# Performance work log

Hardware: AMD Instinct MI355X
Metric: run time of the kernel (lower is better)

Reference implementation:

```python
import jax, jax.numpy as jnp
import numpy as np

B, S, D, H, DH = 2, 2048, 1024, 16, 64

def setup_inputs() -> dict:
    key = jax.random.key(0)
    ks = jax.random.split(key, 9)
    sc = 0.02
    return {
        "x":  jax.random.normal(ks[0], (B, S, D), jnp.float32),
        "Wq": jax.random.normal(ks[1], (H, D, DH), jnp.float32) * sc,
        "bq": jax.random.normal(ks[2], (H, DH), jnp.float32) * sc,
        "Wk": jax.random.normal(ks[3], (H, D, DH), jnp.float32) * sc,
        "bk": jax.random.normal(ks[4], (H, DH), jnp.float32) * sc,
        "Wv": jax.random.normal(ks[5], (H, D, DH), jnp.float32) * sc,
        "bv": jax.random.normal(ks[6], (H, DH), jnp.float32) * sc,
        "Wo": jax.random.normal(ks[7], (D, D), jnp.float32) * sc,
        "bo": jax.random.normal(ks[8], (D,), jnp.float32) * sc,
    }

def reference(x, Wq, bq, Wk, bk, Wv, bv, Wo, bo):
    # Fused version of the per-head Python loop: all H heads batched.
    # q,k,v: [B,H,S,DH]
    q = jnp.einsum("bsi,hid->bhsd", x, Wq) + bq[None, :, None, :]
    k = jnp.einsum("bsi,hid->bhsd", x, Wk) + bk[None, :, None, :]
    v = jnp.einsum("bsi,hid->bhsd", x, Wv) + bv[None, :, None, :]
    scale = 1.0 / jnp.sqrt(jnp.asarray(DH, x.dtype))
    scores = jnp.einsum("bhsd,bhtd->bhst", q, k) * scale  # [B,H,S,S]
    attn = jax.nn.softmax(scores, axis=-1)
    o = jnp.einsum("bhst,bhtd->bhsd", attn, v)            # [B,H,S,DH]
    # torch.cat([head_0,...,head_{H-1}], dim=-1) -> [B,S,H*DH]
    o = jnp.transpose(o, (0, 2, 1, 3)).reshape(B, S, H * DH)
    # Dropout is identity in eval mode; final dense projection.
    return jnp.einsum("bsi,io->bso", o, Wo) + bo
```

## Files before the change

### kernel.cpp

```cpp
#include <hip/hip_runtime.h>
#include <hip/hip_bf16.h>

#define BB 2
#define SS 2048
#define DD 1024
#define HH 16
#define DHH 64

typedef __attribute__((ext_vector_type(8))) __bf16 bf16x8;
typedef __attribute__((ext_vector_type(4))) float f32x4;
typedef __attribute__((ext_vector_type(16))) float f32x16;
typedef __attribute__((ext_vector_type(4))) int i32x4;
typedef __attribute__((ext_vector_type(4))) unsigned int u32x4;

#define MFMA16 __builtin_amdgcn_mfma_f32_16x16x32_bf16
#define MFMA32 __builtin_amdgcn_mfma_f32_32x32x16_bf16

__device__ __forceinline__ unsigned short f2b(float f) {
  __hip_bfloat16 h = __float2bfloat16(f);
  unsigned short u;
  __builtin_memcpy(&u, &h, 2);
  return u;
}

__device__ __forceinline__ float b2f(unsigned short u) {
  unsigned int x = ((unsigned int)u) << 16;
  float f;
  __builtin_memcpy(&f, &x, 4);
  return f;
}

__device__ __forceinline__ float exp2_fast(float x) {
  float r;
  asm("v_exp_f32 %0, %1" : "=v"(r) : "v"(x));
  return r;
}

__device__ __forceinline__ unsigned int cvtpk_bf16(float lo_, float hi_) {
  unsigned int r;
  asm("v_cvt_pk_bf16_f32 %0, %1, %2" : "=v"(r) : "v"(lo_), "v"(hi_));
  return r;
}

__device__ __forceinline__ void gl_lds16(const void* g, void* l) {
  __builtin_amdgcn_global_load_lds((const __attribute__((address_space(1))) void*)g,
                                   (__attribute__((address_space(3))) void*)l, 16, 0, 0);
}

__global__ __launch_bounds__(256) void k_prep(const float* __restrict__ x,
                                              const float* __restrict__ Wq,
                                              const float* __restrict__ Wk,
                                              const float* __restrict__ Wv,
                                              const float* __restrict__ Wo,
                                              unsigned short* __restrict__ xb,
                                              unsigned short* __restrict__ wqkvt,
                                              unsigned short* __restrict__ wot) {
  int blk = blockIdx.x;
  if (blk < 4096) {
    int i = blk * 256 + threadIdx.x;
    float4 v = ((const float4*)x)[i];
    ushort4 o;
    o.x = f2b(v.x); o.y = f2b(v.y); o.z = f2b(v.z); o.w = f2b(v.w);
    ((ushort4*)xb)[i] = o;
    return;
  }
  __shared__ float t[32][33];
  const float* im;
  unsigned short* om;
  int R, C, c0, r0;
  if (blk < 7168) {
    int bi2 = blk - 4096;
    int z = bi2 >> 6, rem = bi2 & 63;
    im = (z < 16 ? Wq : (z < 32 ? Wk : Wv)) + (size_t)(z & 15) * DD * DHH;
    om = wqkvt + (size_t)z * DD * DHH;
    R = DD; C = DHH;
    c0 = (rem & 1) * 32; r0 = (rem >> 1) * 32;
  } else {
    int bi2 = blk - 7168;
    im = Wo; om = wot;
    R = DD; C = DD;
    c0 = (bi2 & 31) * 32; r0 = (bi2 >> 5) * 32;
  }
  int tx = threadIdx.x & 31, ty = threadIdx.x >> 5;
#pragma unroll
  for (int rr = ty; rr < 32; rr += 8)
    t[rr][tx] = im[(size_t)(r0 + rr) * C + c0 + tx];
  __syncthreads();
#pragma unroll
  for (int rr = ty; rr < 32; rr += 8)
    om[(size_t)(c0 + rr) * R + r0 + tx] = f2b(t[tx][rr]);
}

__global__ __launch_bounds__(256) void k_qkv(const unsigned short* __restrict__ A,
                                             const unsigned short* __restrict__ Wt,
                                             const float* __restrict__ bq,
                                             const float* __restrict__ bk,
                                             const float* __restrict__ bv,
                                             unsigned short* __restrict__ Qb,
                                             unsigned short* __restrict__ Kb,
                                             unsigned short* __restrict__ Vtb) {
  __shared__ __align__(16) unsigned short SMEM[2 * 12288];
  int tid = threadIdx.x;
  int w = tid >> 6, l = tid & 63, lr = l & 15, lg = l >> 4;
  int col0 = blockIdx.x * 64, row0 = blockIdx.y * 128;
  int sel = col0 >> 10;
  bool vsel = (sel == 2);
  const float* biasp = sel == 0 ? bq : (sel == 1 ? bk : bv);
  unsigned short* outp = sel == 0 ? Qb : Kb;
  float qscale = sel == 0 ? 0.18033688011112042f : 1.0f;

  int r8 = l >> 3, c8 = l & 7;
  const unsigned short* Ab = A + (size_t)(row0 + w * 32 + r8) * DD + c8 * 8;
  const unsigned short* Bb = Wt + (size_t)(col0 + w * 16 + r8) * DD + c8 * 8;

  f32x4 zero = {0.f, 0.f, 0.f, 0.f};
  f32x4 acc[2][4];
#pragma unroll
  for (int m = 0; m < 2; m++)
#pragma unroll
    for (int n = 0; n < 4; n++) acc[m][n] = zero;

#define QKV_STAGE(T) do { \
    unsigned short* buf_ = SMEM + ((T) & 1) * 12288; \
    int k0_ = (T) * 64; \
    _Pragma("unroll") \
    for (int c = 0; c < 4; c++) \
      gl_lds16(Ab + (size_t)c * 8 * DD + k0_, (char*)buf_ + (w * 32 + c * 8) * 128); \
    _Pragma("unroll") \
    for (int c = 0; c < 2; c++) \
      gl_lds16(Bb + (size_t)c * 8 * DD + k0_, (char*)(buf_ + 8192) + (w * 16 + c * 8) * 128); \
  } while (0)

  QKV_STAGE(0);
  __syncthreads();

  for (int t = 0; t < 16; t++) {
    const unsigned short* As = SMEM + (t & 1) * 12288;
    const unsigned short* Bs = As + 8192;
    if (t + 1 < 16) QKV_STAGE(t + 1);
#pragma unroll
    for (int kk = 0; kk < 2; kk++) {
      bf16x8 af[2], bfr[4];
#pragma unroll
      for (int m = 0; m < 2; m++)
        af[m] = *(const bf16x8*)&As[(w * 32 + m * 16 + lr) * 64 + kk * 32 + lg * 8];
#pragma unroll
      for (int n = 0; n < 4; n++)
        bfr[n] = *(const bf16x8*)&Bs[(n * 16 + lr) * 64 + kk * 32 + lg * 8];
      if (!vsel) {
#pragma unroll
        for (int m = 0; m < 2; m++)
#pragma unroll
          for (int n = 0; n < 4; n++)
            acc[m][n] = MFMA16(af[m], bfr[n], acc[m][n], 0, 0, 0);
      } else {
#pragma unroll
        for (int m = 0; m < 2; m++)
#pragma unroll
          for (int n = 0; n < 4; n++)
            acc[m][n] = MFMA16(bfr[n], af[m], acc[m][n], 0, 0, 0);
      }
    }
    __syncthreads();
  }
#undef QKV_STAGE

  unsigned short* Ts = SMEM;
  if (!vsel) {
#pragma unroll
    for (int n = 0; n < 4; n++) {
      int cl = n * 16 + lr;
      float bias = biasp[(col0 + cl) & 1023];
#pragma unroll
      for (int m = 0; m < 2; m++) {
#pragma unroll
        for (int j = 0; j < 4; j++) {
          int sl = w * 32 + m * 16 + lg * 4 + j;
          Ts[sl * 72 + cl] = f2b((acc[m][n][j] + bias) * qscale);
        }
      }
    }
    __syncthreads();
    int trow = tid >> 3, tc = tid & 7;
#pragma unroll
    for (int pass = 0; pass < 4; pass++) {
      int sl = pass * 32 + trow;
      int c0l = tc * 8;
      i32x4 v = *(const i32x4*)&Ts[sl * 72 + c0l];
      int c = col0 + c0l;
      int hh = (c >> 6) & 15, d = c & 63;
      int row = row0 + sl;
      int b = row >> 11, s = row & 2047;
      *(i32x4*)(outp + ((size_t)(b * HH + hh) * SS + s) * DHH + d) = v;
    }
  } else {
#pragma unroll
    for (int n = 0; n < 4; n++) {
#pragma unroll
      for (int j = 0; j < 4; j++) {
        int cl = n * 16 + lg * 4 + j;
        float bias = bv[((col0 & 1023) + cl) & 1023];
#pragma unroll
        for (int m = 0; m < 2; m++) {
          int sl = w * 32 + m * 16 + lr;
          Ts[cl * 136 + sl] = f2b(acc[m][n][j] + bias);
        }
      }
    }
    __syncthreads();
    int trow = tid >> 4, tc = tid & 15;
    int b = row0 >> 11, s0 = row0 & 2047;
#pragma unroll
    for (int pass = 0; pass < 4; pass++) {
      int cl = pass * 16 + trow;
      int s8 = tc * 8;
      i32x4 v = *(const i32x4*)&Ts[cl * 136 + s8];
      int cg = (col0 & 1023) + cl;
      *(i32x4*)(Vtb + (size_t)(b * 1024 + cg) * SS + s0 + s8) = v;
    }
  }
}

__global__ __launch_bounds__(256) void k_proj(const unsigned short* __restrict__ A,
                                              const unsigned short* __restrict__ Wt,
                                              const float* __restrict__ bo,
                                              float* __restrict__ out) {
  __shared__ __align__(16) unsigned short SMEM[2 * 8192];
  int tid = threadIdx.x;
  int w = tid >> 6, l = tid & 63, lr = l & 15, lg = l >> 4;
  int col0 = blockIdx.x * 64, row0 = blockIdx.y * 64;

  int r8 = l >> 3, c8 = l & 7;
  const unsigned short* Ab = A + (size_t)(row0 + w * 16 + r8) * DD + c8 * 8;
  const unsigned short* Bb = Wt + (size_t)(col0 + w * 16 + r8) * DD + c8 * 8;

  f32x4 zero = {0.f, 0.f, 0.f, 0.f};
  f32x4 acc[4];
#pragma unroll
  for (int n = 0; n < 4; n++) acc[n] = zero;

#define PROJ_STAGE(T) do { \
    unsigned short* buf_ = SMEM + ((T) & 1) * 8192; \
    int k0_ = (T) * 64; \
    _Pragma("unroll") \
    for (int c = 0; c < 2; c++) { \
      gl_lds16(Ab + (size_t)c * 8 * DD + k0_, (char*)buf_ + (w * 16 + c * 8) * 128); \
      gl_lds16(Bb + (size_t)c * 8 * DD + k0_, (char*)(buf_ + 4096) + (w * 16 + c * 8) * 128); \
    } \
  } while (0)

  PROJ_STAGE(0);
  __syncthreads();

  for (int t = 0; t < 16; t++) {
    const unsigned short* As = SMEM + (t & 1) * 8192;
    const unsigned short* Bs = As + 4096;
    if (t + 1 < 16) PROJ_STAGE(t + 1);
#pragma unroll
    for (int kk = 0; kk < 2; kk++) {
      bf16x8 af = *(const bf16x8*)&As[(w * 16 + lr) * 64 + kk * 32 + lg * 8];
      bf16x8 bfr[4];
#pragma unroll
      for (int n = 0; n < 4; n++)
        bfr[n] = *(const bf16x8*)&Bs[(n * 16 + lr) * 64 + kk * 32 + lg * 8];
#pragma unroll
      for (int n = 0; n < 4; n++)
        acc[n] = MFMA16(af, bfr[n], acc[n], 0, 0, 0);
    }
    __syncthreads();
  }
#undef PROJ_STAGE

#pragma unroll
  for (int n = 0; n < 4; n++) {
    int c = col0 + n * 16 + lr;
    float bias = bo[c];
#pragma unroll
    for (int j = 0; j < 4; j++) {
      int row = row0 + w * 16 + lg * 4 + j;
      out[(size_t)row * DD + c] = acc[n][j] + bias;
    }
  }
}

#define QT 128
#define KVB 64

__global__ __launch_bounds__(256, 4) void k_attn(const unsigned short* __restrict__ Q,
                                                 const unsigned short* __restrict__ K,
                                                 const unsigned short* __restrict__ Vt,
                                                 unsigned short* __restrict__ Opart,
                                                 float* __restrict__ lse) {
  __shared__ __align__(16) char sm[32768];

  int tid = threadIdx.x;
  int w = tid >> 6, lane = tid & 63;
  int q32 = lane & 31, hi = lane >> 5;
  int r8 = lane >> 3, c8 = lane & 7;
  int cg = c8 ^ r8;

  int n = blockIdx.x;
  int bh = ((n & 7) << 2) | ((n >> 3) & 3);
  int rest = n >> 5;
  int q0 = (rest & 15) * QT;
  int chunk = rest >> 4;
  int kvbase = chunk * (SS / 2);

  const unsigned short* Qm = Q + (size_t)bh * SS * DHH;
  const unsigned short* Km = K + (size_t)bh * SS * DHH;
  const unsigned short* Vm = Vt + (size_t)bh * DHH * SS;

  bf16x8 qf[4];
  {
    const unsigned short* qrow = Qm + (size_t)(q0 + w * 32 + q32) * DHH + hi * 8;
#pragma unroll
    for (int ks = 0; ks < 4; ks++)
      qf[ks] = *(const bf16x8*)(qrow + ks * 16);
  }

#pragma unroll
  for (int c = 0; c < 2; c++) {
    int rr = w * 16 + c * 8 + r8;
    gl_lds16(Km + (size_t)(kvbase + rr) * DHH + cg * 8, sm + (w * 16 + c * 8) * 128);
    gl_lds16(Vm + (size_t)rr * SS + kvbase + cg * 8, sm + 16384 + (w * 16 + c * 8) * 128);
  }
  __syncthreads();

  f32x16 oacc0 = {}, oacc1 = {};
  float m_ = -1e30f, l_ = 0.f;
  const int swq = (q32 & 7) << 4;

  for (int t = 0; t < SS / 2 / KVB; t++) {
    const char* Kc = sm + (t & 1) * 8192;
    const char* Vc = sm + 16384 + (t & 1) * 8192;

    if (t + 1 < SS / 2 / KVB) {
      int kv0 = kvbase + (t + 1) * KVB;
      char* kd = sm + ((t + 1) & 1) * 8192;
      char* vd = sm + 16384 + ((t + 1) & 1) * 8192;
#pragma unroll
      for (int c = 0; c < 2; c++) {
        int rr = w * 16 + c * 8 + r8;
        gl_lds16(Km + (size_t)(kv0 + rr) * DHH + cg * 8, kd + (w * 16 + c * 8) * 128);
        gl_lds16(Vm + (size_t)rr * SS + kv0 + cg * 8, vd + (w * 16 + c * 8) * 128);
      }
    }

    f32x16 p0 = {}, p1 = {};
    __builtin_amdgcn_s_setprio(1);
#pragma unroll
    for (int ks = 0; ks < 4; ks++) {
      int co = (ks * 32 + hi * 16) ^ swq;
      bf16x8 kf0 = *(const bf16x8*)(Kc + q32 * 128 + co);
      bf16x8 kf1 = *(const bf16x8*)(Kc + (32 + q32) * 128 + co);
      p0 = MFMA32(kf0, qf[ks], p0, 0, 0, 0);
      p1 = MFMA32(kf1, qf[ks], p1, 0, 0, 0);
    }
    __builtin_amdgcn_s_setprio(0);

    float t8[8];
#pragma unroll
    for (int r = 0; r < 8; r++)
      t8[r] = fmaxf(fmaxf(p0[r], p0[r + 8]), fmaxf(p1[r], p1[r + 8]));
#pragma unroll
    for (int r = 0; r < 4; r++) t8[r] = fmaxf(t8[r], t8[r + 4]);
    float tmax = fmaxf(fmaxf(t8[0], t8[1]), fmaxf(t8[2], t8[3]));
    tmax = fmaxf(tmax, __shfl_xor(tmax, 32));

    if (__any(tmax > m_ + 8.0f)) {
      float nm = fmaxf(m_, tmax);
      float al = exp2_fast(m_ - nm);
      m_ = nm; l_ *= al;
#pragma unroll
      for (int r = 0; r < 16; r++) { oacc0[r] *= al; oacc1[r] *= al; }
    }

#pragma unroll
    for (int r = 0; r < 16; r++) p0[r] = exp2_fast(p0[r] - m_);
#pragma unroll
    for (int r = 0; r < 16; r++) p1[r] = exp2_fast(p1[r] - m_);
    float s8[8];
#pragma unroll
    for (int r = 0; r < 8; r++) s8[r] = (p0[r] + p0[r + 8]) + (p1[r] + p1[r + 8]);
#pragma unroll
    for (int r = 0; r < 4; r++) s8[r] += s8[r + 4];
    l_ += ((s8[0] + s8[1]) + (s8[2] + s8[3]));

    __builtin_amdgcn_s_setprio(1);
    u32x4 pa;
#define MKPA(PB, u) do { \
    unsigned int a0 = cvtpk_bf16(PB[8*(u)+0], PB[8*(u)+1]); \
    unsigned int a1 = cvtpk_bf16(PB[8*(u)+2], PB[8*(u)+3]); \
    unsigned int b0 = cvtpk_bf16(PB[8*(u)+4], PB[8*(u)+5]); \
    unsigned int b1 = cvtpk_bf16(PB[8*(u)+6], PB[8*(u)+7]); \
    asm("v_permlane32_swap_b32 %0, %1" : "+v"(a0), "+v"(b0)); \
    asm("v_permlane32_swap_b32 %0, %1" : "+v"(a1), "+v"(b1)); \
    pa[0] = a0; pa[1] = a1; pa[2] = b0; pa[3] = b1; \
  } while (0)
#define PVSTEP(s) do { \
    bf16x8 pf = *(bf16x8*)&pa; \
    bf16x8 vf0 = *(const bf16x8*)(Vc + q32 * 128 + (((s) * 32 + hi * 16) ^ swq)); \
    bf16x8 vf1 = *(const bf16x8*)(Vc + (32 + q32) * 128 + (((s) * 32 + hi * 16) ^ swq)); \
    oacc0 = MFMA32(vf0, pf, oacc0, 0, 0, 0); \
    oacc1 = MFMA32(vf1, pf, oacc1, 0, 0, 0); \
  } while (0)
    MKPA(p0, 0); PVSTEP(0);
    MKPA(p0, 1); PVSTEP(1);
    MKPA(p1, 0); PVSTEP(2);
    MKPA(p1, 1); PVSTEP(3);
#undef MKPA
#undef PVSTEP
    __builtin_amdgcn_s_setprio(0);

    __syncthreads();
  }

  l_ += __shfl_xor(l_, 32);
  float invl = 1.0f / l_;
  float lsev = m_ + __log2f(l_);
  __syncthreads();
  unsigned short* Os = (unsigned short*)sm;
  int rowq = w * 32 + q32;
#pragma unroll
  for (int r = 0; r < 16; r++) {
    int d = (r & 3) + 8 * (r >> 2) + 4 * hi;
    Os[rowq * 72 + d] = f2b(oacc0[r] * invl);
    Os[rowq * 72 + 32 + d] = f2b(oacc1[r] * invl);
  }
  if (hi == 0) lse[((size_t)chunk * 32 + bh) * SS + q0 + rowq] = lsev;
  __syncthreads();
#pragma unroll
  for (int i = 0; i < 4; i++) {
    int ci = tid + i * 256;
    int r = ci >> 3, c = ci & 7;
    i32x4 v = *(const i32x4*)&Os[r * 72 + c * 8];
    *(i32x4*)(Opart + (((size_t)chunk * 32 + bh) * SS + q0 + r) * DHH + c * 8) = v;
  }
}

__global__ __launch_bounds__(256) void k_comb(const unsigned short* __restrict__ Opart,
                                              const float* __restrict__ lse,
                                              unsigned short* __restrict__ Ocat) {
  int g = blockIdx.x * 256 + threadIdx.x;
  int row = g >> 3;
  int d8 = (g & 7) * 8;
  int bh = row >> 11, q = row & 2047;
  int bi = bh >> 4, h = bh & 15;
  float e0 = lse[row], e1 = lse[BB * HH * SS + row];
  float mx = fmaxf(e0, e1);
  float w0 = exp2_fast(e0 - mx), w1 = exp2_fast(e1 - mx);
  float inv = 1.0f / (w0 + w1);
  w0 *= inv; w1 *= inv;
  const unsigned short* P0 = Opart + (size_t)row * DHH + d8;
  const unsigned short* P1 = P0 + (size_t)BB * HH * SS * DHH;
  ushort4 a0 = *(const ushort4*)P0, a1 = *(const ushort4*)(P0 + 4);
  ushort4 b0 = *(const ushort4*)P1, b1 = *(const ushort4*)(P1 + 4);
  ushort4 o0, o1;
  o0.x = f2b(w0 * b2f(a0.x) + w1 * b2f(b0.x));
  o0.y = f2b(w0 * b2f(a0.y) + w1 * b2f(b0.y));
  o0.z = f2b(w0 * b2f(a0.z) + w1 * b2f(b0.z));
  o0.w = f2b(w0 * b2f(a0.w) + w1 * b2f(b0.w));
  o1.x = f2b(w0 * b2f(a1.x) + w1 * b2f(b1.x));
  o1.y = f2b(w0 * b2f(a1.y) + w1 * b2f(b1.y));
  o1.z = f2b(w0 * b2f(a1.z) + w1 * b2f(b1.z));
  o1.w = f2b(w0 * b2f(a1.w) + w1 * b2f(b1.w));
  unsigned short* op = Ocat + ((size_t)(bi * SS + q)) * DD + h * DHH + d8;
  *(ushort4*)op = o0;
  *(ushort4*)(op + 4) = o1;
}

extern "C" void kernel_launch(void* const* d_in, const int* in_sizes, int n_in,
                              void* d_out, int out_size, void* d_ws, size_t ws_size,
                              hipStream_t stream) {
  const float* x  = (const float*)d_in[0];
  const float* Wq = (const float*)d_in[1];
  const float* bq = (const float*)d_in[2];
  const float* Wk = (const float*)d_in[3];
  const float* bk = (const float*)d_in[4];
  const float* Wv = (const float*)d_in[5];
  const float* bv = (const float*)d_in[6];
  const float* Wo = (const float*)d_in[7];
  const float* bo = (const float*)d_in[8];
  float* out = (float*)d_out;

  char* ws = (char*)d_ws;
  unsigned short* xb    = (unsigned short*)(ws);
  unsigned short* wqkvt = (unsigned short*)(ws + (size_t)(8u  << 20));
  unsigned short* wot   = (unsigned short*)(ws + (size_t)(14u << 20));
  unsigned short* Qb    = (unsigned short*)(ws + (size_t)(16u << 20));
  unsigned short* Kb    = (unsigned short*)(ws + (size_t)(24u << 20));
  unsigned short* Vt    = (unsigned short*)(ws + (size_t)(32u << 20));
  unsigned short* Ocat  = (unsigned short*)(ws + (size_t)(40u << 20));
  unsigned short* Opart = (unsigned short*)(ws + (size_t)(48u << 20));
  float*          lse   = (float*)(ws + (size_t)(64u << 20));

  k_prep<<<8192, 256, 0, stream>>>(x, Wq, Wk, Wv, Wo, xb, wqkvt, wot);
  k_qkv<<<dim3(3 * DD / 64, BB * SS / 128), 256, 0, stream>>>(xb, wqkvt, bq, bk, bv, Qb, Kb, Vt);
  k_attn<<<dim3(1024), 256, 0, stream>>>(Qb, Kb, Vt, Opart, lse);
  k_comb<<<dim3(2048), 256, 0, stream>>>(Opart, lse, Ocat);
  k_proj<<<dim3(DD / 64, BB * SS / 64), 256, 0, stream>>>(Ocat, wot, bo, out);
}
```

Measured before the change: 126.2 us.

## Triple-buffer QKV and output projection GEMMs with one barrier per k-step

Converts the QKV and output projection GEMM mainloops from double to triple LDS buffering. Global-to-LDS loads are issued two stages ahead, and partial vmcnt waits let the newest stage stay in flight, so each iteration needs a single barrier instead of two syncs. This is meant to hide global load latency and cut synchronisation stalls. The cost is more LDS per block, with occupancy hints of 2 and 3 added to the launch bounds, and correctness now relies on the hand-written vmcnt counts matching the number of loads per stage.

```diff
diff --git a/kernel.cpp b/kernel.cpp
--- a/kernel.cpp
+++ b/kernel.cpp
@@ -91,15 +91,15 @@
     om[(size_t)(c0 + rr) * R + r0 + tx] = f2b(t[tx][rr]);
 }
 
-__global__ __launch_bounds__(256) void k_qkv(const unsigned short* __restrict__ A,
-                                             const unsigned short* __restrict__ Wt,
-                                             const float* __restrict__ bq,
-                                             const float* __restrict__ bk,
-                                             const float* __restrict__ bv,
-                                             unsigned short* __restrict__ Qb,
-                                             unsigned short* __restrict__ Kb,
-                                             unsigned short* __restrict__ Vtb) {
-  __shared__ __align__(16) unsigned short SMEM[2 * 12288];
+__global__ __launch_bounds__(256, 2) void k_qkv(const unsigned short* __restrict__ A,
+                                                const unsigned short* __restrict__ Wt,
+                                                const float* __restrict__ bq,
+                                                const float* __restrict__ bk,
+                                                const float* __restrict__ bv,
+                                                unsigned short* __restrict__ Qb,
+                                                unsigned short* __restrict__ Kb,
+                                                unsigned short* __restrict__ Vtb) {
+  __shared__ __align__(16) unsigned short SMEM[3 * 12288];
   int tid = threadIdx.x;
   int w = tid >> 6, l = tid & 63, lr = l & 15, lg = l >> 4;
   int col0 = blockIdx.x * 64, row0 = blockIdx.y * 128;
@@ -121,7 +121,7 @@
     for (int n = 0; n < 4; n++) acc[m][n] = zero;
 
 #define QKV_STAGE(T) do { \
-    unsigned short* buf_ = SMEM + ((T) & 1) * 12288; \
+    unsigned short* buf_ = SMEM + ((T) % 3) * 12288; \
     int k0_ = (T) * 64; \
     _Pragma("unroll") \
     for (int c = 0; c < 4; c++) \
@@ -131,40 +131,49 @@
       gl_lds16(Bb + (size_t)c * 8 * DD + k0_, (char*)(buf_ + 8192) + (w * 16 + c * 8) * 128); \
   } while (0)
 
+#define QKV_COMPUTE(T) do { \
+    const unsigned short* As_ = SMEM + ((T) % 3) * 12288; \
+    const unsigned short* Bs_ = As_ + 8192; \
+    _Pragma("unroll") \
+    for (int kk = 0; kk < 2; kk++) { \
+      bf16x8 af[2], bfr[4]; \
+      _Pragma("unroll") \
+      for (int m = 0; m < 2; m++) \
+        af[m] = *(const bf16x8*)&As_[(w * 32 + m * 16 + lr) * 64 + kk * 32 + lg * 8]; \
+      _Pragma("unroll") \
+      for (int n = 0; n < 4; n++) \
+        bfr[n] = *(const bf16x8*)&Bs_[(n * 16 + lr) * 64 + kk * 32 + lg * 8]; \
+      if (!vsel) { \
+        _Pragma("unroll") \
+        for (int m = 0; m < 2; m++) \
+          _Pragma("unroll") \
+          for (int n = 0; n < 4; n++) \
+            acc[m][n] = MFMA16(af[m], bfr[n], acc[m][n], 0, 0, 0); \
+      } else { \
+        _Pragma("unroll") \
+        for (int m = 0; m < 2; m++) \
+          _Pragma("unroll") \
+          for (int n = 0; n < 4; n++) \
+            acc[m][n] = MFMA16(bfr[n], af[m], acc[m][n], 0, 0, 0); \
+      } \
+    } \
+  } while (0)
+
   QKV_STAGE(0);
+  QKV_STAGE(1);
+  for (int t = 0; t < 15; t++) {
+    asm volatile("s_waitcnt vmcnt(6) lgkmcnt(0)" ::: "memory");
+    __builtin_amdgcn_s_barrier();
+    if (t + 2 < 16) QKV_STAGE(t + 2);
+    QKV_COMPUTE(t);
+  }
+  asm volatile("s_waitcnt vmcnt(0) lgkmcnt(0)" ::: "memory");
+  __builtin_amdgcn_s_barrier();
+  QKV_COMPUTE(15);
+#undef QKV_STAGE
+#undef QKV_COMPUTE
+
   __syncthreads();
-
-  for (int t = 0; t < 16; t++) {
-    const unsigned short* As = SMEM + (t & 1) * 12288;
-    const unsigned short* Bs = As + 8192;
-    if (t + 1 < 16) QKV_STAGE(t + 1);
-#pragma unroll
-    for (int kk = 0; kk < 2; kk++) {
-      bf16x8 af[2], bfr[4];
-#pragma unroll
-      for (int m = 0; m < 2; m++)
-        af[m] = *(const bf16x8*)&As[(w * 32 + m * 16 + lr) * 64 + kk * 32 + lg * 8];
-#pragma unroll
-      for (int n = 0; n < 4; n++)
-        bfr[n] = *(const bf16x8*)&Bs[(n * 16 + lr) * 64 + kk * 32 + lg * 8];
-      if (!vsel) {
-#pragma unroll
-        for (int m = 0; m < 2; m++)
-#pragma unroll
-          for (int n = 0; n < 4; n++)
-            acc[m][n] = MFMA16(af[m], bfr[n], acc[m][n], 0, 0, 0);
-      } else {
-#pragma unroll
-        for (int m = 0; m < 2; m++)
-#pragma unroll
-          for (int n = 0; n < 4; n++)
-            acc[m][n] = MFMA16(bfr[n], af[m], acc[m][n], 0, 0, 0);
-      }
-    }
-    __syncthreads();
-  }
-#undef QKV_STAGE
-
   unsigned short* Ts = SMEM;
   if (!vsel) {
 #pragma unroll
@@ -221,11 +230,11 @@
   }
 }
 
-__global__ __launch_bounds__(256) void k_proj(const unsigned short* __restrict__ A,
-                                              const unsigned short* __restrict__ Wt,
-                                              const float* __restrict__ bo,
-                                              float* __restrict__ out) {
-  __shared__ __align__(16) unsigned short SMEM[2 * 8192];
+__global__ __launch_bounds__(256, 3) void k_proj(const unsigned short* __restrict__ A,
+                                                 const unsigned short* __restrict__ Wt,
+                                                 const float* __restrict__ bo,
+                                                 float* __restrict__ out) {
+  __shared__ __align__(16) unsigned short SMEM[3 * 8192];
   int tid = threadIdx.x;
   int w = tid >> 6, l = tid & 63, lr = l & 15, lg = l >> 4;
   int col0 = blockIdx.x * 64, row0 = blockIdx.y * 64;
@@ -240,7 +249,7 @@
   for (int n = 0; n < 4; n++) acc[n] = zero;
 
 #define PROJ_STAGE(T) do { \
-    unsigned short* buf_ = SMEM + ((T) & 1) * 8192; \
+    unsigned short* buf_ = SMEM + ((T) % 3) * 8192; \
     int k0_ = (T) * 64; \
     _Pragma("unroll") \
     for (int c = 0; c < 2; c++) { \
@@ -249,27 +258,35 @@
     } \
   } while (0)
 
+#define PROJ_COMPUTE(T) do { \
+    const unsigned short* As_ = SMEM + ((T) % 3) * 8192; \
+    const unsigned short* Bs_ = As_ + 4096; \
+    _Pragma("unroll") \
+    for (int kk = 0; kk < 2; kk++) { \
+      bf16x8 af = *(const bf16x8*)&As_[(w * 16 + lr) * 64 + kk * 32 + lg * 8]; \
+      bf16x8 bfr[4]; \
+      _Pragma("unroll") \
+      for (int n = 0; n < 4; n++) \
+        bfr[n] = *(const bf16x8*)&Bs_[(n * 16 + lr) * 64 + kk * 32 + lg * 8]; \
+      _Pragma("unroll") \
+      for (int n = 0; n < 4; n++) \
+        acc[n] = MFMA16(af, bfr[n], acc[n], 0, 0, 0); \
+    } \
+  } while (0)
+
   PROJ_STAGE(0);
-  __syncthreads();
-
-  for (int t = 0; t < 16; t++) {
-    const unsigned short* As = SMEM + (t & 1) * 8192;
-    const unsigned short* Bs = As + 4096;
-    if (t + 1 < 16) PROJ_STAGE(t + 1);
-#pragma unroll
-    for (int kk = 0; kk < 2; kk++) {
-      bf16x8 af = *(const bf16x8*)&As[(w * 16 + lr) * 64 + kk * 32 + lg * 8];
-      bf16x8 bfr[4];
-#pragma unroll
-      for (int n = 0; n < 4; n++)
-        bfr[n] = *(const bf16x8*)&Bs[(n * 16 + lr) * 64 + kk * 32 + lg * 8];
-#pragma unroll
-      for (int n = 0; n < 4; n++)
-        acc[n] = MFMA16(af, bfr[n], acc[n], 0, 0, 0);
-    }
-    __syncthreads();
-  }
+  PROJ_STAGE(1);
+  for (int t = 0; t < 15; t++) {
+    asm volatile("s_waitcnt vmcnt(4) lgkmcnt(0)" ::: "memory");
+    __builtin_amdgcn_s_barrier();
+    if (t + 2 < 16) PROJ_STAGE(t + 2);
+    PROJ_COMPUTE(t);
+  }
+  asm volatile("s_waitcnt vmcnt(0) lgkmcnt(0)" ::: "memory");
+  __builtin_amdgcn_s_barrier();
+  PROJ_COMPUTE(15);
 #undef PROJ_STAGE
+#undef PROJ_COMPUTE
 
 #pragma unroll
   for (int n = 0; n < 4; n++) {
```

Result: slower. 130.2 us, median of 2 (+3.1%).
